# Kernel optimization log

Measured on AMD Instinct MI355X. Metric: run time of the kernel, lower is better.

## Reference

```python
import jax, jax.numpy as jnp
import numpy as np

NEG_INF = -9e15  # matches the source's -9000000000000000.0 mask fill
ALPHA = 0.2      # leaky_relu negative slope


def setup_inputs() -> dict:
    key = jax.random.key(0)
    k1, k2, k3, k4 = jax.random.split(key, 4)
    B, N, C_IN, C_OUT, H = 2, 2048, 128, 128, 16
    c = C_OUT // H  # 8 per-head features; equals H//2 so source's a-slice is consistent
    node_feats = jax.random.normal(k1, (B, N, C_IN), dtype=jnp.float32)
    # random 0/1 adjacency with self-loops
    adj = jax.random.randint(k2, (B, N, N), 0, 2).astype(jnp.float32)
    adj = jnp.maximum(adj, jnp.eye(N, dtype=jnp.float32)[None])
    # glorot-uniform-ish params
    W = jax.random.normal(k3, (C_IN, H * c), dtype=jnp.float32) * np.sqrt(2.0 / (C_IN + H * c))
    b = jnp.zeros((H * c,), dtype=jnp.float32)
    a = jax.random.normal(k4, (H, 2 * c), dtype=jnp.float32) * np.sqrt(2.0 / (H + 2 * c))
    return {"node_feats": node_feats, "adj_matrix": adj, "W": W, "b": b, "a": a}


def reference(node_feats, adj_matrix, W, b, a):
    B, N = node_feats.shape[:2]
    H = a.shape[0]
    c = a.shape[1] // 2
    # projection + split into heads: [B, N, H, c]
    h = (node_feats @ W + b).reshape(B, N, H, c)
    # additive attention halves (source slices a along last axis)
    logit_parent = jnp.einsum('bnhc,hc->bnh', h, a[:, :c])
    logit_child = jnp.einsum('bnhc,hc->bnh', h, a[:, c:])
    # dense broadcast-add logits: [B, N(i), N(j), H]
    attn_logits = logit_parent[:, :, None, :] + logit_child[:, None, :, :]
    attn_logits = jax.nn.leaky_relu(attn_logits, negative_slope=ALPHA)
    attn_logits = jnp.where(adj_matrix[..., None] == 1.0, attn_logits, NEG_INF)
    attn_probs = jax.nn.softmax(attn_logits, axis=2)  # over source nodes j
    out = jnp.einsum('bijh,bjhc->bihc', attn_probs, h)
    out = out.reshape(B, N, H * c)  # concat_heads=True
    return out, adj_matrix
```

## Files before the change

### kernel.cpp

```cpp
#include <hip/hip_runtime.h>
#include <hip/hip_bf16.h>


#define B_   2
#define N_   2048
#define CIN_ 128
#define H_   16

typedef _Float16 h2  __attribute__((ext_vector_type(2)));
typedef _Float16 v8h __attribute__((ext_vector_type(8)));
typedef float    v4f __attribute__((ext_vector_type(4)));

#define SC6 0.015625f

__device__ inline h2 pk_f16(float a, float b) {
  return __builtin_bit_cast(h2, __builtin_amdgcn_cvt_pkrtz(a, b));
}
__device__ inline unsigned as_u32(h2 v) { return __builtin_bit_cast(unsigned, v); }
__device__ inline h2 as_h2(unsigned u) { return __builtin_bit_cast(h2, u); }

__device__ inline unsigned mask4(float4 f) {
  unsigned r = (unsigned)f.x | ((unsigned)f.y << 8) |
               ((unsigned)f.z << 16) | ((unsigned)f.w << 24);
  return (r << 8) - r;
}

__global__ __launch_bounds__(128) void proj_kernel(
    const float* __restrict__ nf, const float* __restrict__ W,
    const float* __restrict__ bias, const float* __restrict__ a,
    unsigned* __restrict__ hQ, unsigned* __restrict__ qI,
    float* __restrict__ lpT, unsigned* __restrict__ ones) {
  const int row0 = blockIdx.x * 4;
  const int t    = threadIdx.x;
  if (blockIdx.x == 0) {
    ones[t] = 0x3C003C00u; ones[t + 128] = 0x3C003C00u;
    ones[t + 256] = 0x3C003C00u; ones[t + 384] = 0x3C003C00u;
  }
  __shared__ float sNf[4][CIN_];
  ((float4*)&sNf[0][0])[t] = ((const float4*)(nf + (long)row0 * CIN_))[t];
  __syncthreads();
  float acc[4];
  const float bv = bias[t];
#pragma unroll
  for (int r = 0; r < 4; ++r) acc[r] = bv;
#pragma unroll 8
  for (int k = 0; k < CIN_; ++k) {
    const float w = W[k * 128 + t];
#pragma unroll
    for (int r = 0; r < 4; ++r) acc[r] = fmaf(sNf[r][k], w, acc[r]);
  }
  const int h = t >> 3, kc = t & 7;
  const int b = row0 >> 11, n0 = row0 & (N_ - 1);
  const int bh = b * H_ + h;
  const int cdw = n0 >> 1;
  uint2 hv;
  hv.x = as_u32(pk_f16(acc[0], acc[1]));
  hv.y = as_u32(pk_f16(acc[2], acc[3]));
  *(uint2*)(hQ + ((long)(bh * 8 + kc)) * (N_ / 2) + cdw) = hv;

  const float ap = a[h * 16 + kc], ac = a[h * 16 + 8 + kc];
  float lpv[4], lcv[4];
#pragma unroll
  for (int r = 0; r < 4; ++r) {
    float x = acc[r] * ap, y = acc[r] * ac;
#pragma unroll
    for (int s = 1; s < 8; s <<= 1) {
      x += __shfl_xor(x, s);
      y += __shfl_xor(y, s);
    }
    lpv[r] = x; lcv[r] = y;
  }
  if (kc == 0) {
    float4 l0 = {lpv[0], lpv[1], lpv[2], lpv[3]};
    *(float4*)(lpT + (long)bh * N_ + n0) = l0;
    uint2 q1, q2;
    q1.x = as_u32(pk_f16(__expf(lcv[0]) * SC6, __expf(lcv[1]) * SC6));
    q1.y = as_u32(pk_f16(__expf(lcv[2]) * SC6, __expf(lcv[3]) * SC6));
    q2.x = as_u32(pk_f16(__expf(0.2f * lcv[0]) * SC6, __expf(0.2f * lcv[1]) * SC6));
    q2.y = as_u32(pk_f16(__expf(0.2f * lcv[2]) * SC6, __expf(0.2f * lcv[3]) * SC6));
    const int addr = bh * 2048 + (cdw >> 4) * 32 + ((cdw >> 2) & 3) * 8;
    const int off  = cdw & 3;
    *(uint2*)(qI + addr + off)     = q1;
    *(uint2*)(qI + addr + 4 + off) = q2;
  }
}

__global__ __launch_bounds__(256, 4) void attn_kernel(
    const float* __restrict__ adj, const unsigned* __restrict__ hQ,
    const unsigned* __restrict__ qI, const float* __restrict__ lpT,
    const unsigned* __restrict__ ones, float* __restrict__ out,
    float* __restrict__ adj_out) {
  const int L    = (blockIdx.x & 7) * 128 + (blockIdx.x >> 3);
  const int hg   = L & 3;
  const int it   = (L >> 2) & 127;
  const int b    = L >> 9;
  const int i0   = it * 16;
  const int t    = threadIdx.x;
  const int w    = t >> 6;
  const int lane = t & 63;
  const int m    = lane & 15;
  const int q    = lane >> 4;
  const int h    = hg * 4 + w;
  const int bh   = b * H_ + h;

  __shared__ uint2 sAm[1024];

  const int  tm = t & 15, cg = t >> 4;
  const int  chl = cg >> 1, qh = (cg & 1) * 2;
  const long abase = ((long)(b * N_) + i0 + tm) * N_ + cg * 16;
  const bool owner_even = (hg == 0) | (hg == 1) | (hg == 2) | (hg == 3);

  float4 f0, f1, f2, f3;
  auto STAGE_LOAD = [&](int ss) {
    const float* ap = adj + abase + ss * 256;
    f0 = *(const float4*)(ap);
    f1 = *(const float4*)(ap + 4);
    f2 = *(const float4*)(ap + 8);
    f3 = *(const float4*)(ap + 12);
  };
  auto STAGE_WRITE = [&](int ss) {
    const int buf = (ss & 1) * 512;
    uint2 mv0; mv0.x = mask4(f0); mv0.y = mask4(f1);
    uint2 mv1; mv1.x = mask4(f2); mv1.y = mask4(f3);
    sAm[buf + chl * 64 + qh * 16 + tm]       = mv0;
    sAm[buf + chl * 64 + (qh + 1) * 16 + tm] = mv1;
    if (hg == (ss & 3)) {
      float* op = adj_out + abase + ss * 256;
      *(float4*)(op)      = f0;
      *(float4*)(op + 4)  = f1;
      *(float4*)(op + 8)  = f2;
      *(float4*)(op + 12) = f3;
    }
  };

  const float lp  = lpT[(long)bh * N_ + i0 + m];
  const float e1  = __expf(lp) * SC6, e2 = __expf(0.2f * lp) * SC6;
  const h2 P1 = pk_f16(e1, e1), P2 = pk_f16(e2, e2);

  const unsigned* qp = qI + bh * 2048 + q * 8;
  const unsigned hmask = (m < 8) ? ~0u : 0u;
  const unsigned* hp = (m < 8)
      ? hQ + ((long)(bh * 8 + m)) * (N_ / 2) + q * 4
      : ones + q * 4;

  uint4 bq1[2], bq2[2], bhq[2];
  bq1[0] = *(const uint4*)(qp);       bq2[0] = *(const uint4*)(qp + 4);
  bq1[1] = *(const uint4*)(qp + 32);  bq2[1] = *(const uint4*)(qp + 36);
  bhq[0] = *(const uint4*)(hp);
  bhq[1] = *(const uint4*)(hp + (16 & hmask));

  v4f acc = {0.f, 0.f, 0.f, 0.f};

  STAGE_LOAD(0);
  STAGE_WRITE(0);
  __syncthreads();

  for (int s = 0; s < 8; ++s) {
    if (s < 7) STAGE_LOAD(s + 1);
    const int buf = (s & 1) * 512;
#pragma unroll
    for (int cc = 0; cc < 8; ++cc) {
      const int ch = s * 8 + cc;
      const int p  = ch & 1;
      const uint4 nq1 = *(const uint4*)(qp + (ch + 2) * 32);
      const uint4 nq2 = *(const uint4*)(qp + (ch + 2) * 32 + 4);
      const uint4 nhq = *(const uint4*)(hp + (((ch + 2) * 16) & hmask));

      const uint2 Mv = sAm[buf + cc * 64 + lane];
      const unsigned ma = __builtin_amdgcn_perm(Mv.x, Mv.x, 0x01010000u);
      const unsigned mb = __builtin_amdgcn_perm(Mv.x, Mv.x, 0x03030202u);
      const unsigned mc = __builtin_amdgcn_perm(Mv.y, Mv.y, 0x01010000u);
      const unsigned md = __builtin_amdgcn_perm(Mv.y, Mv.y, 0x03030202u);

      const uint4 q1 = bq1[p], q2 = bq2[p];
      const v8h bf = __builtin_bit_cast(v8h, bhq[p]);
      const uint4 af = {
        as_u32(__builtin_elementwise_max(P1 * as_h2(q1.x), P2 * as_h2(q2.x))) & ma,
        as_u32(__builtin_elementwise_max(P1 * as_h2(q1.y), P2 * as_h2(q2.y))) & mb,
        as_u32(__builtin_elementwise_max(P1 * as_h2(q1.z), P2 * as_h2(q2.z))) & mc,
        as_u32(__builtin_elementwise_max(P1 * as_h2(q1.w), P2 * as_h2(q2.w))) & md};
      acc = __builtin_amdgcn_mfma_f32_16x16x32_f16(
          __builtin_bit_cast(v8h, af), bf, acc, 0, 0, 0);

      bq1[p] = nq1; bq2[p] = nq2; bhq[p] = nhq;
    }
    if (s < 7) { STAGE_WRITE(s + 1); __syncthreads(); }
  }

#pragma unroll
  for (int r = 0; r < 4; ++r) {
    const float sden = __shfl(acc[r], (lane & 48) | 8);
    if (m < 8) {
      const long gi = ((long)(b * N_ + i0 + q * 4 + r)) * H_ + h;
      out[gi * 8 + m] = acc[r] / sden;
    }
  }
  (void)owner_even;
}

extern "C" void kernel_launch(void* const* d_in, const int* in_sizes, int n_in,
                              void* d_out, int out_size, void* d_ws, size_t ws_size,
                              hipStream_t stream) {
  const float* nf   = (const float*)d_in[0];
  const float* adj  = (const float*)d_in[1];
  const float* W    = (const float*)d_in[2];
  const float* bias = (const float*)d_in[3];
  const float* a    = (const float*)d_in[4];

  float* out     = (float*)d_out;
  float* adj_out = out + (long)B_ * N_ * H_ * 8;

  unsigned* ws   = (unsigned*)d_ws;
  unsigned* hQ   = ws;
  unsigned* qI   = ws + 262144;
  float*    lpT  = (float*)(ws + 327680);
  unsigned* ones = ws + 393216;

  hipLaunchKernelGGL(proj_kernel, dim3(B_ * N_ / 4), dim3(128), 0, stream,
                     nf, W, bias, a, hQ, qI, lpT, ones);
  hipLaunchKernelGGL(attn_kernel, dim3(1024), dim3(256), 0,
                     stream, adj, hQ, qI, lpT, ones, out, adj_out);
}
```

Baseline: 146.5 us.

## Split adjacency masking and copy into a separate prep kernel

Adds a prep kernel that reads the fp32 adjacency once, writes the adj_out copy and packs a byte mask into a workspace buffer. The attention kernel then reads the compact mask straight from global memory with a 4-deep register prefetch, so it no longer needs shared memory staging or barriers. This takes the large adjacency read off the MFMA loop's critical path. The cost is an extra kernel launch plus a write and re-read of the mask buffer, and the prep and attention work are no longer overlapped.

```diff
diff --git a/kernel.cpp b/kernel.cpp
--- a/kernel.cpp
+++ b/kernel.cpp
@@ -85,106 +85,87 @@
   }
 }
 
+__global__ __launch_bounds__(256) void prep_kernel(
+    const float* __restrict__ adj, float* __restrict__ adj_out,
+    unsigned* __restrict__ mks) {
+  const int L    = (blockIdx.x & 7) * 128 + (blockIdx.x >> 3);
+  const int oct  = L & 7, it32 = (L >> 3) & 63, b = L >> 9;
+  const int t    = threadIdx.x;
+  const int g    = t & 7, r = t >> 3;
+  const int it16 = it32 * 2 + (r >> 4), m = r & 15;
+  const int q    = g >> 1, half = g & 1;
+  const long rbase = ((long)(b * N_) + it32 * 32 + r) * N_;
+  unsigned* mb = mks + ((long)(b * 128 + it16)) * 8192;
+#pragma unroll
+  for (int c8 = 0; c8 < 8; ++c8) {
+    const int ch  = oct * 8 + c8;
+    const int col = ch * 32 + g * 4;
+    const float4 fa = *(const float4*)(adj + rbase + col);
+    *(float4*)(adj_out + rbase + col) = fa;
+    mb[ch * 128 + (m * 4 + q) * 2 + half] = mask4(fa);
+  }
+}
+
 __global__ __launch_bounds__(256, 4) void attn_kernel(
-    const float* __restrict__ adj, const unsigned* __restrict__ hQ,
-    const unsigned* __restrict__ qI, const float* __restrict__ lpT,
-    const unsigned* __restrict__ ones, float* __restrict__ out,
-    float* __restrict__ adj_out) {
-  const int L    = (blockIdx.x & 7) * 128 + (blockIdx.x >> 3);
-  const int hg   = L & 3;
-  const int it   = (L >> 2) & 127;
-  const int b    = L >> 9;
-  const int i0   = it * 16;
-  const int t    = threadIdx.x;
-  const int w    = t >> 6;
-  const int lane = t & 63;
-  const int m    = lane & 15;
-  const int q    = lane >> 4;
-  const int h    = hg * 4 + w;
-  const int bh   = b * H_ + h;
-
-  __shared__ uint2 sAm[1024];
-
-  const int  tm = t & 15, cg = t >> 4;
-  const int  chl = cg >> 1, qh = (cg & 1) * 2;
-  const long abase = ((long)(b * N_) + i0 + tm) * N_ + cg * 16;
-  const bool owner_even = (hg == 0) | (hg == 1) | (hg == 2) | (hg == 3);
-
-  float4 f0, f1, f2, f3;
-  auto STAGE_LOAD = [&](int ss) {
-    const float* ap = adj + abase + ss * 256;
-    f0 = *(const float4*)(ap);
-    f1 = *(const float4*)(ap + 4);
-    f2 = *(const float4*)(ap + 8);
-    f3 = *(const float4*)(ap + 12);
-  };
-  auto STAGE_WRITE = [&](int ss) {
-    const int buf = (ss & 1) * 512;
-    uint2 mv0; mv0.x = mask4(f0); mv0.y = mask4(f1);
-    uint2 mv1; mv1.x = mask4(f2); mv1.y = mask4(f3);
-    sAm[buf + chl * 64 + qh * 16 + tm]       = mv0;
-    sAm[buf + chl * 64 + (qh + 1) * 16 + tm] = mv1;
-    if (hg == (ss & 3)) {
-      float* op = adj_out + abase + ss * 256;
-      *(float4*)(op)      = f0;
-      *(float4*)(op + 4)  = f1;
-      *(float4*)(op + 8)  = f2;
-      *(float4*)(op + 12) = f3;
-    }
-  };
-
-  const float lp  = lpT[(long)bh * N_ + i0 + m];
-  const float e1  = __expf(lp) * SC6, e2 = __expf(0.2f * lp) * SC6;
+    const unsigned* __restrict__ hQ, const unsigned* __restrict__ qI,
+    const float* __restrict__ lpT, const unsigned* __restrict__ ones,
+    const unsigned* __restrict__ mks, float* __restrict__ out) {
+  const int L  = (blockIdx.x & 7) * 128 + (blockIdx.x >> 3);
+  const int hg = L & 3, it = (L >> 2) & 127, b = L >> 9;
+  const int i0 = it * 16;
+  const int t = threadIdx.x, w = t >> 6, lane = t & 63;
+  const int m = lane & 15, q = lane >> 4;
+  const int h = hg * 4 + w, bh = b * H_ + h;
+
+  const float lp = lpT[(long)bh * N_ + i0 + m];
+  const float e1 = __expf(lp) * SC6, e2 = __expf(0.2f * lp) * SC6;
   const h2 P1 = pk_f16(e1, e1), P2 = pk_f16(e2, e2);
 
+  const uint2* mp = (const uint2*)mks + ((long)(b * 128 + it)) * 4096 + (m * 4 + q);
   const unsigned* qp = qI + bh * 2048 + q * 8;
   const unsigned hmask = (m < 8) ? ~0u : 0u;
   const unsigned* hp = (m < 8)
       ? hQ + ((long)(bh * 8 + m)) * (N_ / 2) + q * 4
       : ones + q * 4;
 
-  uint4 bq1[2], bq2[2], bhq[2];
-  bq1[0] = *(const uint4*)(qp);       bq2[0] = *(const uint4*)(qp + 4);
-  bq1[1] = *(const uint4*)(qp + 32);  bq2[1] = *(const uint4*)(qp + 36);
-  bhq[0] = *(const uint4*)(hp);
-  bhq[1] = *(const uint4*)(hp + (16 & hmask));
+  uint2 bmk[4];
+  uint4 bq1[4], bq2[4], bhq[4];
+#pragma unroll
+  for (int d = 0; d < 4; ++d) {
+    bmk[d] = mp[d * 64];
+    bq1[d] = *(const uint4*)(qp + d * 32);
+    bq2[d] = *(const uint4*)(qp + d * 32 + 4);
+    bhq[d] = *(const uint4*)(hp + ((d * 16) & hmask));
+  }
 
   v4f acc = {0.f, 0.f, 0.f, 0.f};
 
-  STAGE_LOAD(0);
-  STAGE_WRITE(0);
-  __syncthreads();
-
-  for (int s = 0; s < 8; ++s) {
-    if (s < 7) STAGE_LOAD(s + 1);
-    const int buf = (s & 1) * 512;
-#pragma unroll
-    for (int cc = 0; cc < 8; ++cc) {
-      const int ch = s * 8 + cc;
-      const int p  = ch & 1;
-      const uint4 nq1 = *(const uint4*)(qp + (ch + 2) * 32);
-      const uint4 nq2 = *(const uint4*)(qp + (ch + 2) * 32 + 4);
-      const uint4 nhq = *(const uint4*)(hp + (((ch + 2) * 16) & hmask));
-
-      const uint2 Mv = sAm[buf + cc * 64 + lane];
-      const unsigned ma = __builtin_amdgcn_perm(Mv.x, Mv.x, 0x01010000u);
-      const unsigned mb = __builtin_amdgcn_perm(Mv.x, Mv.x, 0x03030202u);
-      const unsigned mc = __builtin_amdgcn_perm(Mv.y, Mv.y, 0x01010000u);
-      const unsigned md = __builtin_amdgcn_perm(Mv.y, Mv.y, 0x03030202u);
-
-      const uint4 q1 = bq1[p], q2 = bq2[p];
-      const v8h bf = __builtin_bit_cast(v8h, bhq[p]);
-      const uint4 af = {
-        as_u32(__builtin_elementwise_max(P1 * as_h2(q1.x), P2 * as_h2(q2.x))) & ma,
-        as_u32(__builtin_elementwise_max(P1 * as_h2(q1.y), P2 * as_h2(q2.y))) & mb,
-        as_u32(__builtin_elementwise_max(P1 * as_h2(q1.z), P2 * as_h2(q2.z))) & mc,
-        as_u32(__builtin_elementwise_max(P1 * as_h2(q1.w), P2 * as_h2(q2.w))) & md};
-      acc = __builtin_amdgcn_mfma_f32_16x16x32_f16(
-          __builtin_bit_cast(v8h, af), bf, acc, 0, 0, 0);
-
-      bq1[p] = nq1; bq2[p] = nq2; bhq[p] = nhq;
-    }
-    if (s < 7) { STAGE_WRITE(s + 1); __syncthreads(); }
+#pragma unroll
+  for (int ch = 0; ch < 64; ++ch) {
+    const int p = ch & 3, f = (ch + 4) & 63;
+    const uint2 nmk = mp[f * 64];
+    const uint4 nq1 = *(const uint4*)(qp + f * 32);
+    const uint4 nq2 = *(const uint4*)(qp + f * 32 + 4);
+    const uint4 nhq = *(const uint4*)(hp + ((f * 16) & hmask));
+    __builtin_amdgcn_sched_barrier(0);
+
+    const uint2 Mv = bmk[p];
+    const unsigned ma = __builtin_amdgcn_perm(Mv.x, Mv.x, 0x01010000u);
+    const unsigned mb = __builtin_amdgcn_perm(Mv.x, Mv.x, 0x03030202u);
+    const unsigned mc = __builtin_amdgcn_perm(Mv.y, Mv.y, 0x01010000u);
+    const unsigned md = __builtin_amdgcn_perm(Mv.y, Mv.y, 0x03030202u);
+
+    const uint4 q1 = bq1[p], q2 = bq2[p];
+    const v8h bf = __builtin_bit_cast(v8h, bhq[p]);
+    const uint4 af = {
+      as_u32(__builtin_elementwise_max(P1 * as_h2(q1.x), P2 * as_h2(q2.x))) & ma,
+      as_u32(__builtin_elementwise_max(P1 * as_h2(q1.y), P2 * as_h2(q2.y))) & mb,
+      as_u32(__builtin_elementwise_max(P1 * as_h2(q1.z), P2 * as_h2(q2.z))) & mc,
+      as_u32(__builtin_elementwise_max(P1 * as_h2(q1.w), P2 * as_h2(q2.w))) & md};
+    acc = __builtin_amdgcn_mfma_f32_16x16x32_f16(
+        __builtin_bit_cast(v8h, af), bf, acc, 0, 0, 0);
+
+    bmk[p] = nmk; bq1[p] = nq1; bq2[p] = nq2; bhq[p] = nhq;
   }
 
 #pragma unroll
@@ -195,7 +176,6 @@
       out[gi * 8 + m] = acc[r] / sden;
     }
   }
-  (void)owner_even;
 }
 
 extern "C" void kernel_launch(void* const* d_in, const int* in_sizes, int n_in,
@@ -215,9 +195,12 @@
   unsigned* qI   = ws + 262144;
   float*    lpT  = (float*)(ws + 327680);
   unsigned* ones = ws + 393216;
+  unsigned* mks  = ws + 393728;
 
   hipLaunchKernelGGL(proj_kernel, dim3(B_ * N_ / 4), dim3(128), 0, stream,
                      nf, W, bias, a, hQ, qI, lpT, ones);
-  hipLaunchKernelGGL(attn_kernel, dim3(1024), dim3(256), 0,
-                     stream, adj, hQ, qI, lpT, ones, out, adj_out);
-}
+  hipLaunchKernelGGL(prep_kernel, dim3(1024), dim3(256), 0, stream,
+                     adj, adj_out, mks);
+  hipLaunchKernelGGL(attn_kernel, dim3(1024), dim3(256), 0, stream,
+                     hQ, qI, lpT, ones, mks, out);
+}
```

Result: slower. 171.9 us (+17.3%).
